# Optimization experiments

Measured on AMD Instinct MI355X. Metric: run time of the kernel, lower is better.

Reference implementation:

```python
import jax, jax.numpy as jnp
import numpy as np
import math

C = 512
NUM_HEADS = 4
GROUPS = 32  # group_count(512, 32)
EPS = 1e-5


def group_norm(x, gamma, beta):
    # x: [b, c, h, w]; normalize over (c//GROUPS, h, w) per group
    b, c, h, w = x.shape
    xg = x.reshape(b, GROUPS, -1)
    mu = jnp.mean(xg, axis=-1, keepdims=True)
    var = jnp.var(xg, axis=-1, keepdims=True)
    xn = ((xg - mu) * jax.lax.rsqrt(var + EPS)).reshape(b, c, h, w)
    return xn * gamma[None, :, None, None] + beta[None, :, None, None]


def setup_inputs() -> dict:
    key = jax.random.key(0)
    ks = jax.random.split(key, 5)
    b, h, w = 2, 64, 64
    x = jax.random.normal(ks[0], (b, C, h, w), dtype=jnp.float32)
    gn_w = jnp.ones((C,), dtype=jnp.float32)
    gn_b = jnp.zeros((C,), dtype=jnp.float32)
    s_qkv = 1.0 / math.sqrt(C)
    w_qkv = jax.random.uniform(ks[1], (3 * C, C), jnp.float32, -s_qkv, s_qkv)
    b_qkv = jax.random.uniform(ks[2], (3 * C,), jnp.float32, -s_qkv, s_qkv)
    w_proj = jax.random.uniform(ks[3], (C, C), jnp.float32, -s_qkv, s_qkv)
    b_proj = jax.random.uniform(ks[4], (C,), jnp.float32, -s_qkv, s_qkv)
    return {"x": x, "gn_w": gn_w, "gn_b": gn_b, "w_qkv": w_qkv,
            "b_qkv": b_qkv, "w_proj": w_proj, "b_proj": b_proj}


def reference(x, gn_w, gn_b, w_qkv, b_qkv, w_proj, b_proj):
    b, c, h, w = x.shape
    L = h * w
    nh = NUM_HEADS
    hd = c // nh
    residual = x
    xn = group_norm(x, gn_w, gn_b).reshape(b, c, L)
    # Conv1d with kernel_size=1 == channelwise linear: [b, 3c, L]
    qkv = jnp.einsum('bcl,oc->bol', xn, w_qkv) + b_qkv[None, :, None]
    q, k, v = jnp.split(qkv, 3, axis=1)
    q = q.reshape(b, nh, hd, L)
    k = k.reshape(b, nh, hd, L)
    v = v.reshape(b, nh, hd, L)
    scores = jnp.einsum('bncd,bnce->bnde', q, k) / math.sqrt(hd)
    attn = jax.nn.softmax(scores, axis=-1)
    out = jnp.einsum('bnde,bnce->bncd', attn, v).reshape(b, c, L)
    out = jnp.einsum('bcl,oc->bol', out, w_proj) + b_proj[None, :, None]
    return out.reshape(b, c, h, w) + residual
```

## Files before the change

kernel.cpp:

```cpp
#include <hip/hip_runtime.h>
#include <math.h>

typedef __bf16 bf16;
typedef __bf16 bf16x8 __attribute__((ext_vector_type(8)));
typedef __bf16 bf16x4 __attribute__((ext_vector_type(4)));
typedef float f32x4 __attribute__((ext_vector_type(4)));

#define QSCALE (0.08838834764831845f * 1.4426950408889634f)

__device__ __forceinline__ void gll16(const bf16* g, bf16* l) {
    __builtin_amdgcn_global_load_lds((const __attribute__((address_space(1))) void*)g,
                                     (__attribute__((address_space(3))) void*)l, 16, 0, 0);
}

__global__ void k_pre(const float* __restrict__ wqkv, const float* __restrict__ wproj,
                      const float* __restrict__ x,
                      bf16* __restrict__ wqkv_b, bf16* __restrict__ wproj_b,
                      float* __restrict__ part) {
    int blk = blockIdx.x;
    if (blk < 1024) {
        int i = blk * 256 + threadIdx.x;
        const int n1 = (1536 * 512) / 4;
        float4 v;
        bf16* dst;
        if (i < n1) { v = ((const float4*)wqkv)[i];      dst = wqkv_b + (size_t)i * 4; }
        else        { v = ((const float4*)wproj)[i - n1]; dst = wproj_b + (size_t)(i - n1) * 4; }
        bf16x4 o;
        o[0] = (bf16)v.x; o[1] = (bf16)v.y; o[2] = (bf16)v.z; o[3] = (bf16)v.w;
        *(bf16x4*)dst = o;
        return;
    }
    int b2 = blk - 1024;
    int grp = b2 >> 2, p = b2 & 3;
    const float4* src = (const float4*)(x + (size_t)grp * 65536 + (size_t)p * 16384);
    float s = 0.f, ss = 0.f;
    for (int it = 0; it < 16; ++it) {
        float4 v = src[threadIdx.x + it * 256];
        s  += v.x + v.y + v.z + v.w;
        ss += v.x * v.x + v.y * v.y + v.z * v.z + v.w * v.w;
    }
    for (int off = 32; off; off >>= 1) { s += __shfl_down(s, off); ss += __shfl_down(ss, off); }
    __shared__ float rs[4], rss[4];
    int wave = threadIdx.x >> 6;
    if ((threadIdx.x & 63) == 0) { rs[wave] = s; rss[wave] = ss; }
    __syncthreads();
    if (threadIdx.x == 0) {
        part[(grp * 4 + p) * 2]     = rs[0] + rs[1] + rs[2] + rs[3];
        part[(grp * 4 + p) * 2 + 1] = rss[0] + rss[1] + rss[2] + rss[3];
    }
}

__global__ __launch_bounds__(256) void k_gn_norm_t(const float* __restrict__ x, const float* __restrict__ gw,
                                                   const float* __restrict__ gb, const float* __restrict__ part,
                                                   bf16* __restrict__ xn_t) {
    __shared__ float sX[64 * 69];
    __shared__ float sMean[4], sRstd[4];
    int b = blockIdx.z, c0 = blockIdx.y * 64, l0 = blockIdx.x * 64;
    int t = threadIdx.x;
    if (t < 4) {
        int g = b * 32 + (c0 >> 4) + t;
        float S = 0.f, SS = 0.f;
        for (int p = 0; p < 4; ++p) { S += part[(g * 4 + p) * 2]; SS += part[(g * 4 + p) * 2 + 1]; }
        float mean = S * (1.f / 65536.f);
        float var  = SS * (1.f / 65536.f) - mean * mean;
        sMean[t] = mean;
        sRstd[t] = rsqrtf(var + 1e-5f);
    }
    __syncthreads();
    int cr = t >> 4, lq = t & 15;
    const float* xp = x + ((size_t)(b * 512 + c0)) * 4096 + l0;
    for (int i = 0; i < 4; ++i) {
        int c = cr + i * 16;
        int cg = c0 + c;
        float mean = sMean[c >> 4], rstd = sRstd[c >> 4];
        float ga = gw[cg] * rstd;
        float be = gb[cg] - mean * ga;
        float4 v = *(const float4*)(xp + (size_t)c * 4096 + lq * 4);
        float* d = &sX[c * 69 + lq * 4];
        d[0] = v.x * ga + be; d[1] = v.y * ga + be; d[2] = v.z * ga + be; d[3] = v.w * ga + be;
    }
    __syncthreads();
    int lr = t >> 3, cp = t & 7;
    bf16* dst = xn_t + ((size_t)b * 4096 + l0) * 512 + c0;
    for (int i = 0; i < 2; ++i) {
        int l = lr + i * 32;
        bf16x8 o;
        for (int j = 0; j < 8; ++j) o[j] = (bf16)sX[(cp * 8 + j) * 69 + l];
        *(bf16x8*)(dst + (size_t)l * 512 + cp * 8) = o;
    }
}

template<int BM>
__global__ __launch_bounds__(256) void k_gemm(
    const bf16* __restrict__ A, size_t aStride, const bf16* __restrict__ B, size_t bStride,
    const float* __restrict__ bias_m, const float* __restrict__ bias_n,
    bf16* __restrict__ outb, float* __restrict__ outf, const float* __restrict__ resid,
    int ldo, size_t oStride, float qscale, int qthresh) {
    constexpr int MT = BM / 32;
    constexpr int NA = BM / 32;
    constexpr int BUF = (BM + 128) * 64;
    __shared__ bf16 smem[2 * BUF];
    int bz = blockIdx.z;
    int m0 = blockIdx.y * BM, n0 = blockIdx.x * 128;
    int tid = threadIdx.x, lane = tid & 63, wave = tid >> 6;
    int lo = lane & 15, quad = lane >> 4;
    int lr = lane >> 3, ls = lane & 7;
    int mw = (wave >> 1) * (BM / 2), nw = (wave & 1) * 64;
    const bf16* aptr[NA];
    int adst[NA];
    for (int i = 0; i < NA; ++i) {
        int r0 = wave * (BM / 4) + i * 8;
        int row = r0 + lr;
        aptr[i] = A + (size_t)bz * aStride + (size_t)(m0 + row) * 512 + ((ls ^ (row & 7)) * 8);
        adst[i] = r0 * 64;
    }
    const bf16* bptr[4];
    int bdst[4];
    for (int i = 0; i < 4; ++i) {
        int r0 = wave * 32 + i * 8;
        int row = r0 + lr;
        bptr[i] = B + (size_t)bz * bStride + (size_t)(n0 + row) * 512 + ((ls ^ (row & 7)) * 8);
        bdst[i] = BM * 64 + r0 * 64;
    }
    f32x4 acc[MT][4] = {};
    for (int i = 0; i < NA; ++i) { gll16(aptr[i], &smem[adst[i]]); aptr[i] += 64; }
    for (int i = 0; i < 4;  ++i) { gll16(bptr[i], &smem[bdst[i]]); bptr[i] += 64; }
    for (int step = 0; step < 8; ++step) {
        int cur = step & 1;
        __syncthreads();
        if (step < 7) {
            bf16* nb = &smem[(cur ^ 1) * BUF];
            for (int i = 0; i < NA; ++i) { gll16(aptr[i], nb + adst[i]); aptr[i] += 64; }
            for (int i = 0; i < 4;  ++i) { gll16(bptr[i], nb + bdst[i]); bptr[i] += 64; }
        }
        const bf16* sA = &smem[cur * BUF];
        const bf16* sB = sA + BM * 64;
        for (int kk = 0; kk < 2; ++kk) {
            bf16x8 af[MT], bfr[4];
            int sw = ((kk * 4 + quad) ^ (lo & 7)) * 8;
            for (int t = 0; t < MT; ++t) af[t]  = *(const bf16x8*)&sA[(mw + t * 16 + lo) * 64 + sw];
            for (int t = 0; t < 4;  ++t) bfr[t] = *(const bf16x8*)&sB[(nw + t * 16 + lo) * 64 + sw];
            for (int mt = 0; mt < MT; ++mt)
                for (int nt = 0; nt < 4; ++nt)
                    acc[mt][nt] = __builtin_amdgcn_mfma_f32_16x16x32_bf16(af[mt], bfr[nt], acc[mt][nt], 0, 0, 0);
        }
    }
    for (int mt = 0; mt < MT; ++mt) {
        int rowb = m0 + mw + mt * 16 + quad * 4;
        for (int nt = 0; nt < 4; ++nt) {
            int col = n0 + nw + nt * 16 + lo;
            float bn = bias_n ? bias_n[col] : 0.f;
            float sc = (col < qthresh) ? qscale : 1.f;
            for (int r = 0; r < 4; ++r) {
                int row = rowb + r;
                float bval = bias_m ? bias_m[row] : bn;
                float v = (acc[mt][nt][r] + bval) * sc;
                size_t idx = (size_t)bz * oStride + (size_t)row * ldo + col;
                if (outf) outf[idx] = v + resid[idx];
                else      outb[idx] = (bf16)v;
            }
        }
    }
}

__global__ __launch_bounds__(512, 2) void k_attn(const bf16* __restrict__ qkT, const bf16* __restrict__ vmat,
                                                 bf16* __restrict__ attnT) {
    __shared__ __align__(16) char smem[104448];
    bf16* sE = (bf16*)smem;
    float* sStat = (float*)(smem + 102400);
    int bidx = blockIdx.x;
    int bh = bidx & 7;
    int bb = bh >> 2, h = bh & 3;
    int l0 = (bidx >> 3) * 128;
    int tid = threadIdx.x, lane = tid & 63, wave = tid >> 6;
    int lo = lane & 15, quad = lane >> 4;
    int a = wave & 3, b2 = wave >> 2;
    int lr16 = lane >> 4, ls16 = lane & 15;
    int lr8 = lane >> 3, ls8 = lane & 7;
    const bf16* qbase = qkT + ((size_t)bb * 4096 + l0) * 1024 + h * 128;
    const bf16* kbase = qkT + (size_t)bb * 4096 * 1024 + 512 + h * 128;
    const bf16* vbase = vmat + (size_t)(bb * 512 + h * 128) * 4096;
    for (int i = 0; i < 4; ++i) {
        int r0 = wave * 16 + i * 4;
        int row = r0 + lr16;
        gll16(qbase + (size_t)row * 1024 + ((ls16 ^ (row & 15)) * 8), sE + r0 * 128);
    }
    __syncthreads();
    bf16x8 qf[2][4];
    for (int nt = 0; nt < 2; ++nt) {
        int row = a * 32 + nt * 16 + lo;
        for (int kk = 0; kk < 4; ++kk)
            qf[nt][kk] = *(const bf16x8*)&sE[row * 128 + (((kk * 4 + quad) ^ lo) * 8)];
    }
    __syncthreads();
    const bf16* kptr[2]; int kdst[2];
    const bf16* vptr[2]; int vdst[2];
    for (int i = 0; i < 2; ++i) {
        int r0 = wave * 8 + i * 4;
        int row = r0 + lr16;
        kptr[i] = kbase + (size_t)row * 1024 + ((ls16 ^ (row & 15)) * 8);
        kdst[i] = r0 * 128;
        int s0 = wave * 16 + i * 8;
        int srow = s0 + lr8;
        vptr[i] = vbase + (size_t)srow * 4096 + ((ls8 ^ (srow & 7)) * 8);
        vdst[i] = s0 * 64;
    }
    bf16* sPe = (bf16*)(smem + 65536) + wave * 1280;
    float l_r[2];
    l_r[0] = l_r[1] = 0.f;
    f32x4 oacc[8][2] = {};
    for (int i = 0; i < 2; ++i) { gll16(kptr[i], sE + kdst[i]); kptr[i] += (size_t)64 * 1024; }
    for (int i = 0; i < 2; ++i) { gll16(vptr[i], sE + 16384 + vdst[i]); vptr[i] += 64; }
    for (int it = 0; it < 64; ++it) {
        int cur = it & 1;
        __syncthreads();
        if (it < 63) {
            bf16* nk = sE + (cur ^ 1) * 8192;
            bf16* nv = sE + 16384 + (cur ^ 1) * 8192;
            for (int i = 0; i < 2; ++i) { gll16(kptr[i], nk + kdst[i]); kptr[i] += (size_t)64 * 1024; }
            for (int i = 0; i < 2; ++i) { gll16(vptr[i], nv + vdst[i]); vptr[i] += 64; }
        }
        const bf16* sK = sE + cur * 8192;
        const bf16* sV = sE + 16384 + cur * 8192;
        f32x4 s[2][2];
        for (int mt = 0; mt < 2; ++mt) {
            int krow = b2 * 32 + mt * 16 + lo;
            bf16x8 kf[4];
            for (int kk = 0; kk < 4; ++kk)
                kf[kk] = *(const bf16x8*)&sK[krow * 128 + (((kk * 4 + quad) ^ lo) * 8)];
            for (int nt = 0; nt < 2; ++nt) {
                f32x4 acc = {};
                for (int kk = 0; kk < 4; ++kk)
                    acc = __builtin_amdgcn_mfma_f32_16x16x32_bf16(kf[kk], qf[nt][kk], acc, 0, 0, 0);
                s[mt][nt] = acc;
            }
        }
        for (int nt = 0; nt < 2; ++nt) {
            float sm = 0.f;
            for (int mt = 0; mt < 2; ++mt) {
                bf16x4 pk;
                for (int r = 0; r < 4; ++r) {
                    float pv = __builtin_amdgcn_exp2f(s[mt][nt][r]);
                    sm += pv;
                    pk[r] = (bf16)pv;
                }
                *(bf16x4*)&sPe[(nt * 16 + lo) * 40 + mt * 16 + quad * 4] = pk;
            }
            sm += __shfl_xor(sm, 16);
            sm += __shfl_xor(sm, 32);
            l_r[nt] += sm;
        }
        bf16x8 pf[2];
        for (int nt = 0; nt < 2; ++nt)
            pf[nt] = *(const bf16x8*)&sPe[(nt * 16 + lo) * 40 + quad * 8];
        for (int mt2 = 0; mt2 < 8; ++mt2) {
            bf16x8 vf = *(const bf16x8*)&sV[(mt2 * 16 + lo) * 64 + (((b2 * 4 + quad) ^ (lo & 7)) * 8)];
            for (int nt = 0; nt < 2; ++nt)
                oacc[mt2][nt] = __builtin_amdgcn_mfma_f32_16x16x32_bf16(vf, pf[nt], oacc[mt2][nt], 0, 0, 0);
        }
    }
    __syncthreads();
    if (quad == 0) {
        for (int nt = 0; nt < 2; ++nt) {
            int qb = a * 32 + nt * 16 + lo;
            sStat[qb * 2 + b2] = l_r[nt];
        }
    }
    __syncthreads();
    float inv[2];
    for (int nt = 0; nt < 2; ++nt) {
        int qb = a * 32 + nt * 16 + lo;
        inv[nt] = 1.f / (sStat[qb * 2] + sStat[qb * 2 + 1]);
    }
    float* sOm = (float*)smem;
    bf16* sOut = (bf16*)(smem + 67584);
    if (b2 == 1) {
        for (int mt2 = 0; mt2 < 8; ++mt2)
            for (int nt = 0; nt < 2; ++nt)
                for (int r = 0; r < 4; ++r) {
                    int vc = mt2 * 16 + quad * 4 + r;
                    sOm[a * 4224 + vc * 33 + nt * 16 + lo] = oacc[mt2][nt][r];
                }
    }
    __syncthreads();
    if (b2 == 0) {
        for (int mt2 = 0; mt2 < 8; ++mt2)
            for (int nt = 0; nt < 2; ++nt)
                for (int r = 0; r < 4; ++r) {
                    int vc = mt2 * 16 + quad * 4 + r;
                    float v = (oacc[mt2][nt][r] + sOm[a * 4224 + vc * 33 + nt * 16 + lo]) * inv[nt];
                    sOut[(a * 32 + nt * 16 + lo) * 136 + vc] = (bf16)v;
                }
    }
    __syncthreads();
    bf16* dst = attnT + ((size_t)bb * 4096 + l0) * 512 + h * 128;
    for (int i = 0; i < 4; ++i) {
        int row = (tid >> 4) + i * 32;
        int chunk = tid & 15;
        bf16x8 v = *(const bf16x8*)&sOut[row * 136 + chunk * 8];
        *(bf16x8*)(dst + (size_t)row * 512 + chunk * 8) = v;
    }
}

extern "C" void kernel_launch(void* const* d_in, const int* in_sizes, int n_in,
                              void* d_out, int out_size, void* d_ws, size_t ws_size,
                              hipStream_t stream) {
    const float* x      = (const float*)d_in[0];
    const float* gn_w   = (const float*)d_in[1];
    const float* gn_b   = (const float*)d_in[2];
    const float* w_qkv  = (const float*)d_in[3];
    const float* b_qkv  = (const float*)d_in[4];
    const float* w_proj = (const float*)d_in[5];
    const float* b_proj = (const float*)d_in[6];
    float* out = (float*)d_out;
    char* ws = (char*)d_ws;
    bf16* wqkv_b  = (bf16*)(ws + 0);
    bf16* wproj_b = (bf16*)(ws + 1572864);
    bf16* xn_t    = (bf16*)(ws + 2097152);
    bf16* qkT     = (bf16*)(ws + 10485760);
    bf16* vb      = (bf16*)(ws + 27262976);
    bf16* attnT   = (bf16*)(ws + 35651584);
    float* part   = (float*)(ws + 44040192);

    k_pre<<<1280, 256, 0, stream>>>(w_qkv, w_proj, x, wqkv_b, wproj_b, part);
    k_gn_norm_t<<<dim3(64, 8, 2), 256, 0, stream>>>(x, gn_w, gn_b, part, xn_t);
    k_gemm<128><<<dim3(8, 32, 2), 256, 0, stream>>>(xn_t, (size_t)4096 * 512, wqkv_b, (size_t)0,
                                                    nullptr, b_qkv, qkT, nullptr, nullptr,
                                                    1024, (size_t)4096 * 1024, QSCALE, 512);
    k_gemm<64><<<dim3(32, 8, 2), 256, 0, stream>>>(wqkv_b + 1024 * 512, (size_t)0, xn_t, (size_t)4096 * 512,
                                                   b_qkv + 1024, nullptr, vb, nullptr, nullptr,
                                                   4096, (size_t)512 * 4096, 1.f, 0);
    k_attn<<<256, 512, 0, stream>>>(qkT, vb, attnT);
    k_gemm<64><<<dim3(32, 8, 2), 256, 0, stream>>>(wproj_b, (size_t)0, attnT, (size_t)4096 * 512,
                                                   b_proj, nullptr, nullptr, out, x,
                                                   4096, (size_t)512 * 4096, 1.f, 0);
}
```

Baseline: 216.9 us.

## Fuse QK and V projection GEMMs with LDS-staged transposed epilogue

The two separate QKV GEMM launches (QK with row-major output and V with transposed operands) become one kernel over all 1536 output columns. Blocks in the V column range transpose their tile through LDS before writing, and all blocks stage output through LDS to make vectorized 16-byte stores. The generic GEMM is also specialized per use with launch_bounds occupancy hints. In attention, the cross-lane row-sum shuffle moves out of the inner loop to run once at the end. This saves a launch and the scalar strided stores, at the cost of extra LDS traffic and a barrier in the epilogue.

```diff
diff --git a/kernel.cpp b/kernel.cpp
--- a/kernel.cpp
+++ b/kernel.cpp
@@ -90,74 +90,146 @@
     }
 }
 
-template<int BM>
-__global__ __launch_bounds__(256) void k_gemm(
-    const bf16* __restrict__ A, size_t aStride, const bf16* __restrict__ B, size_t bStride,
-    const float* __restrict__ bias_m, const float* __restrict__ bias_n,
-    bf16* __restrict__ outb, float* __restrict__ outf, const float* __restrict__ resid,
-    int ldo, size_t oStride, float qscale, int qthresh) {
-    constexpr int MT = BM / 32;
-    constexpr int NA = BM / 32;
-    constexpr int BUF = (BM + 128) * 64;
+__global__ __launch_bounds__(256, 3) void k_gemm_qkv(
+    const bf16* __restrict__ A, const bf16* __restrict__ W, const float* __restrict__ bias,
+    bf16* __restrict__ qkT, bf16* __restrict__ vb) {
+    constexpr int BUF = (64 + 128) * 64;
     __shared__ bf16 smem[2 * BUF];
     int bz = blockIdx.z;
-    int m0 = blockIdx.y * BM, n0 = blockIdx.x * 128;
+    int m0 = blockIdx.y * 64, n0 = blockIdx.x * 128;
     int tid = threadIdx.x, lane = tid & 63, wave = tid >> 6;
     int lo = lane & 15, quad = lane >> 4;
     int lr = lane >> 3, ls = lane & 7;
-    int mw = (wave >> 1) * (BM / 2), nw = (wave & 1) * 64;
-    const bf16* aptr[NA];
-    int adst[NA];
-    for (int i = 0; i < NA; ++i) {
-        int r0 = wave * (BM / 4) + i * 8;
+    int mw = (wave >> 1) * 32, nw = (wave & 1) * 64;
+    const bf16* aptr[2]; int adst[2];
+    for (int i = 0; i < 2; ++i) {
+        int r0 = wave * 16 + i * 8;
         int row = r0 + lr;
-        aptr[i] = A + (size_t)bz * aStride + (size_t)(m0 + row) * 512 + ((ls ^ (row & 7)) * 8);
+        aptr[i] = A + (size_t)bz * (4096 * 512) + (size_t)(m0 + row) * 512 + ((ls ^ (row & 7)) * 8);
         adst[i] = r0 * 64;
     }
-    const bf16* bptr[4];
-    int bdst[4];
+    const bf16* bptr[4]; int bdst[4];
     for (int i = 0; i < 4; ++i) {
         int r0 = wave * 32 + i * 8;
         int row = r0 + lr;
-        bptr[i] = B + (size_t)bz * bStride + (size_t)(n0 + row) * 512 + ((ls ^ (row & 7)) * 8);
-        bdst[i] = BM * 64 + r0 * 64;
-    }
-    f32x4 acc[MT][4] = {};
-    for (int i = 0; i < NA; ++i) { gll16(aptr[i], &smem[adst[i]]); aptr[i] += 64; }
-    for (int i = 0; i < 4;  ++i) { gll16(bptr[i], &smem[bdst[i]]); bptr[i] += 64; }
+        bptr[i] = W + (size_t)(n0 + row) * 512 + ((ls ^ (row & 7)) * 8);
+        bdst[i] = 64 * 64 + r0 * 64;
+    }
+    f32x4 acc[2][4] = {};
+    for (int i = 0; i < 2; ++i) { gll16(aptr[i], &smem[adst[i]]); aptr[i] += 64; }
+    for (int i = 0; i < 4; ++i) { gll16(bptr[i], &smem[bdst[i]]); bptr[i] += 64; }
     for (int step = 0; step < 8; ++step) {
         int cur = step & 1;
         __syncthreads();
         if (step < 7) {
             bf16* nb = &smem[(cur ^ 1) * BUF];
-            for (int i = 0; i < NA; ++i) { gll16(aptr[i], nb + adst[i]); aptr[i] += 64; }
-            for (int i = 0; i < 4;  ++i) { gll16(bptr[i], nb + bdst[i]); bptr[i] += 64; }
+            for (int i = 0; i < 2; ++i) { gll16(aptr[i], nb + adst[i]); aptr[i] += 64; }
+            for (int i = 0; i < 4; ++i) { gll16(bptr[i], nb + bdst[i]); bptr[i] += 64; }
         }
         const bf16* sA = &smem[cur * BUF];
-        const bf16* sB = sA + BM * 64;
+        const bf16* sB = sA + 64 * 64;
         for (int kk = 0; kk < 2; ++kk) {
-            bf16x8 af[MT], bfr[4];
+            bf16x8 af[2], bfr[4];
             int sw = ((kk * 4 + quad) ^ (lo & 7)) * 8;
-            for (int t = 0; t < MT; ++t) af[t]  = *(const bf16x8*)&sA[(mw + t * 16 + lo) * 64 + sw];
-            for (int t = 0; t < 4;  ++t) bfr[t] = *(const bf16x8*)&sB[(nw + t * 16 + lo) * 64 + sw];
-            for (int mt = 0; mt < MT; ++mt)
+            for (int t = 0; t < 2; ++t) af[t]  = *(const bf16x8*)&sA[(mw + t * 16 + lo) * 64 + sw];
+            for (int t = 0; t < 4; ++t) bfr[t] = *(const bf16x8*)&sB[(nw + t * 16 + lo) * 64 + sw];
+            for (int mt = 0; mt < 2; ++mt)
                 for (int nt = 0; nt < 4; ++nt)
                     acc[mt][nt] = __builtin_amdgcn_mfma_f32_16x16x32_bf16(af[mt], bfr[nt], acc[mt][nt], 0, 0, 0);
         }
     }
-    for (int mt = 0; mt < MT; ++mt) {
+    __syncthreads();
+    bf16* sT = smem;
+    bool isv = (n0 >= 1024);
+    float sc = (n0 < 512) ? QSCALE : 1.f;
+    for (int mt = 0; mt < 2; ++mt)
+        for (int nt = 0; nt < 4; ++nt) {
+            int c = nw + nt * 16 + lo;
+            float bv = bias[n0 + c];
+            for (int r = 0; r < 4; ++r) {
+                int l = mw + mt * 16 + quad * 4 + r;
+                float v = (acc[mt][nt][r] + bv) * sc;
+                if (isv) sT[c * 72 + l]  = (bf16)v;
+                else     sT[l * 136 + c] = (bf16)v;
+            }
+        }
+    __syncthreads();
+    if (isv) {
+        bf16* dst = vb + (size_t)bz * (512 * 4096) + (size_t)(n0 - 1024) * 4096 + m0;
+        int c = tid >> 1, h = tid & 1;
+        for (int j = 0; j < 4; ++j) {
+            int ch = h + j * 2;
+            bf16x8 v = *(const bf16x8*)&sT[c * 72 + ch * 8];
+            *(bf16x8*)(dst + (size_t)c * 4096 + ch * 8) = v;
+        }
+    } else {
+        bf16* dst = qkT + (size_t)bz * (4096 * 1024) + (size_t)m0 * 1024 + n0;
+        int l = tid >> 2, h = tid & 3;
+        for (int j = 0; j < 4; ++j) {
+            int ch = h + j * 4;
+            bf16x8 v = *(const bf16x8*)&sT[l * 136 + ch * 8];
+            *(bf16x8*)(dst + (size_t)l * 1024 + ch * 8) = v;
+        }
+    }
+}
+
+__global__ __launch_bounds__(256, 3) void k_gemm_proj(
+    const bf16* __restrict__ W, const bf16* __restrict__ Bm,
+    const float* __restrict__ bias_m,
+    float* __restrict__ outf, const float* __restrict__ resid) {
+    constexpr int BUF = (64 + 128) * 64;
+    __shared__ bf16 smem[2 * BUF];
+    int bz = blockIdx.z;
+    int m0 = blockIdx.y * 64, n0 = blockIdx.x * 128;
+    int tid = threadIdx.x, lane = tid & 63, wave = tid >> 6;
+    int lo = lane & 15, quad = lane >> 4;
+    int lr = lane >> 3, ls = lane & 7;
+    int mw = (wave >> 1) * 32, nw = (wave & 1) * 64;
+    const bf16* aptr[2]; int adst[2];
+    for (int i = 0; i < 2; ++i) {
+        int r0 = wave * 16 + i * 8;
+        int row = r0 + lr;
+        aptr[i] = W + (size_t)(m0 + row) * 512 + ((ls ^ (row & 7)) * 8);
+        adst[i] = r0 * 64;
+    }
+    const bf16* bptr[4]; int bdst[4];
+    for (int i = 0; i < 4; ++i) {
+        int r0 = wave * 32 + i * 8;
+        int row = r0 + lr;
+        bptr[i] = Bm + (size_t)bz * (4096 * 512) + (size_t)(n0 + row) * 512 + ((ls ^ (row & 7)) * 8);
+        bdst[i] = 64 * 64 + r0 * 64;
+    }
+    f32x4 acc[2][4] = {};
+    for (int i = 0; i < 2; ++i) { gll16(aptr[i], &smem[adst[i]]); aptr[i] += 64; }
+    for (int i = 0; i < 4; ++i) { gll16(bptr[i], &smem[bdst[i]]); bptr[i] += 64; }
+    for (int step = 0; step < 8; ++step) {
+        int cur = step & 1;
+        __syncthreads();
+        if (step < 7) {
+            bf16* nb = &smem[(cur ^ 1) * BUF];
+            for (int i = 0; i < 2; ++i) { gll16(aptr[i], nb + adst[i]); aptr[i] += 64; }
+            for (int i = 0; i < 4; ++i) { gll16(bptr[i], nb + bdst[i]); bptr[i] += 64; }
+        }
+        const bf16* sA = &smem[cur * BUF];
+        const bf16* sB = sA + 64 * 64;
+        for (int kk = 0; kk < 2; ++kk) {
+            bf16x8 af[2], bfr[4];
+            int sw = ((kk * 4 + quad) ^ (lo & 7)) * 8;
+            for (int t = 0; t < 2; ++t) af[t]  = *(const bf16x8*)&sA[(mw + t * 16 + lo) * 64 + sw];
+            for (int t = 0; t < 4; ++t) bfr[t] = *(const bf16x8*)&sB[(nw + t * 16 + lo) * 64 + sw];
+            for (int mt = 0; mt < 2; ++mt)
+                for (int nt = 0; nt < 4; ++nt)
+                    acc[mt][nt] = __builtin_amdgcn_mfma_f32_16x16x32_bf16(af[mt], bfr[nt], acc[mt][nt], 0, 0, 0);
+        }
+    }
+    for (int mt = 0; mt < 2; ++mt) {
         int rowb = m0 + mw + mt * 16 + quad * 4;
         for (int nt = 0; nt < 4; ++nt) {
             int col = n0 + nw + nt * 16 + lo;
-            float bn = bias_n ? bias_n[col] : 0.f;
-            float sc = (col < qthresh) ? qscale : 1.f;
             for (int r = 0; r < 4; ++r) {
                 int row = rowb + r;
-                float bval = bias_m ? bias_m[row] : bn;
-                float v = (acc[mt][nt][r] + bval) * sc;
-                size_t idx = (size_t)bz * oStride + (size_t)row * ldo + col;
-                if (outf) outf[idx] = v + resid[idx];
-                else      outb[idx] = (bf16)v;
+                size_t idx = (size_t)bz * (512 * 4096) + (size_t)row * 4096 + col;
+                outf[idx] = acc[mt][nt][r] + bias_m[row] + resid[idx];
             }
         }
     }
@@ -246,8 +318,6 @@
                 }
                 *(bf16x4*)&sPe[(nt * 16 + lo) * 40 + mt * 16 + quad * 4] = pk;
             }
-            sm += __shfl_xor(sm, 16);
-            sm += __shfl_xor(sm, 32);
             l_r[nt] += sm;
         }
         bf16x8 pf[2];
@@ -258,6 +328,10 @@
             for (int nt = 0; nt < 2; ++nt)
                 oacc[mt2][nt] = __builtin_amdgcn_mfma_f32_16x16x32_bf16(vf, pf[nt], oacc[mt2][nt], 0, 0, 0);
         }
+    }
+    for (int nt = 0; nt < 2; ++nt) {
+        l_r[nt] += __shfl_xor(l_r[nt], 16);
+        l_r[nt] += __shfl_xor(l_r[nt], 32);
     }
     __syncthreads();
     if (quad == 0) {
@@ -324,14 +398,7 @@
 
     k_pre<<<1280, 256, 0, stream>>>(w_qkv, w_proj, x, wqkv_b, wproj_b, part);
     k_gn_norm_t<<<dim3(64, 8, 2), 256, 0, stream>>>(x, gn_w, gn_b, part, xn_t);
-    k_gemm<128><<<dim3(8, 32, 2), 256, 0, stream>>>(xn_t, (size_t)4096 * 512, wqkv_b, (size_t)0,
-                                                    nullptr, b_qkv, qkT, nullptr, nullptr,
-                                                    1024, (size_t)4096 * 1024, QSCALE, 512);
-    k_gemm<64><<<dim3(32, 8, 2), 256, 0, stream>>>(wqkv_b + 1024 * 512, (size_t)0, xn_t, (size_t)4096 * 512,
-                                                   b_qkv + 1024, nullptr, vb, nullptr, nullptr,
-                                                   4096, (size_t)512 * 4096, 1.f, 0);
+    k_gemm_qkv<<<dim3(12, 64, 2), 256, 0, stream>>>(xn_t, wqkv_b, b_qkv, qkT, vb);
     k_attn<<<256, 512, 0, stream>>>(qkT, vb, attnT);
-    k_gemm<64><<<dim3(32, 8, 2), 256, 0, stream>>>(wproj_b, (size_t)0, attnT, (size_t)4096 * 512,
-                                                   b_proj, nullptr, nullptr, out, x,
-                                                   4096, (size_t)512 * 4096, 1.f, 0);
-}
+    k_gemm_proj<<<dim3(32, 8, 2), 256, 0, stream>>>(wproj_b, attnT, b_proj, out, x);
+}
```

Measured after the change: 195.6 us. -9.8%, faster.
